# Kernel optimization log

Measured on AMD Instinct MI355X. Metric: run time of the kernel, lower is better.

Reference implementation:

```python
import jax, jax.numpy as jnp
import numpy as np

N = 20000       # nodes
E = 640000      # edges
H = 128         # hidden_nf = input_nf = output_nf = d_model = d_inner (expand=1)
D_STATE = 64
D_CONV = 4
DT_RANK = 8     # ceil(d_model/16) = ceil(128/16)


def setup_inputs() -> dict:
    key = jax.random.key(0)
    ks = jax.random.split(key, 20)
    g = lambda k, shape, s=0.05: jax.random.normal(k, shape, jnp.float32) * s
    return {
        'h': g(ks[0], (N, H), 1.0),
        'coord': g(ks[1], (N, 3), 1.0),
        'edge_index': jax.random.randint(ks[2], (2, E), 0, N),
        # edge_mlp: Linear(2H+1,H) ReLU Linear(H,H) ReLU
        'W_e1': g(ks[3], (H, 2 * H + 1)), 'b_e1': jnp.zeros(H, jnp.float32),
        'W_e2': g(ks[4], (H, H)), 'b_e2': jnp.zeros(H, jnp.float32),
        # att_mlp: Linear(H,1) + sigmoid
        'w_att': g(ks[5], (1, H)), 'b_att': jnp.zeros(1, jnp.float32),
        # node_mlp: Linear(2H,H) ReLU Linear(H,H)
        'W_n1': g(ks[6], (H, 2 * H)), 'b_n1': jnp.zeros(H, jnp.float32),
        'W_n2': g(ks[7], (H, H)), 'b_n2': jnp.zeros(H, jnp.float32),
        # coord_mlp: Linear(H,H) ReLU Linear(H,1,bias=False) (xavier gain 0.001)
        'W_c1': g(ks[8], (H, H)), 'b_c1': jnp.zeros(H, jnp.float32),
        'W_c2': g(ks[9], (1, H), 0.001),
        # pre_norm LayerNorm
        'ln_g': jnp.ones(H, jnp.float32), 'ln_b': jnp.zeros(H, jnp.float32),
        # Mamba(d_model=H, d_state=64, d_conv=4, expand=1)
        'in_proj_w': g(ks[10], (2 * H, H)),
        'conv_w': g(ks[11], (H, D_CONV), 0.2), 'conv_b': jnp.zeros(H, jnp.float32),
        'x_proj_w': g(ks[12], (DT_RANK + 2 * D_STATE, H)),
        'dt_proj_w': g(ks[13], (H, DT_RANK)), 'dt_proj_b': jnp.full((H,), -4.0, jnp.float32),
        'A_log': jnp.log(jnp.broadcast_to(jnp.arange(1, D_STATE + 1, dtype=jnp.float32), (H, D_STATE))),
        'D_skip': jnp.ones(H, jnp.float32),
        'out_proj_w': g(ks[14], (H, H)),
    }


def _layernorm(x, g, b):
    mu = jnp.mean(x, -1, keepdims=True)
    var = jnp.mean((x - mu) ** 2, -1, keepdims=True)
    return (x - mu) / jnp.sqrt(var + 1e-5) * g + b


def _mamba(x, in_proj_w, conv_w, conv_b, x_proj_w, dt_proj_w, dt_proj_b, A_log, D_skip, out_proj_w):
    # x: [L, H] treated as batch-1 sequence
    L = x.shape[0]
    xz = x @ in_proj_w.T                       # [L, 2H]
    u, z = xz[:, :H], xz[:, H:]
    # causal depthwise conv1d, kernel D_CONV
    up = jnp.pad(u, ((D_CONV - 1, 0), (0, 0)))
    uc = conv_b + sum(up[k:k + L] * conv_w[:, k] for k in range(D_CONV))
    uc = jax.nn.silu(uc)                       # [L, H]
    x_dbl = uc @ x_proj_w.T                    # [L, dt_rank + 2*d_state]
    dt = jax.nn.softplus(x_dbl[:, :DT_RANK] @ dt_proj_w.T + dt_proj_b)  # [L, H]
    Bm = x_dbl[:, DT_RANK:DT_RANK + D_STATE]   # [L, d_state]
    Cm = x_dbl[:, DT_RANK + D_STATE:]          # [L, d_state]
    A = -jnp.exp(A_log)                        # [H, d_state]

    def step(s, inp):
        dt_t, b_t, c_t, u_t = inp
        s = jnp.exp(dt_t[:, None] * A) * s + (dt_t * u_t)[:, None] * b_t[None, :]
        y = jnp.sum(s * c_t[None, :], -1) + D_skip * u_t
        return s, y

    _, ys = jax.lax.scan(step, jnp.zeros((H, D_STATE), jnp.float32), (dt, Bm, Cm, uc))
    y = ys * jax.nn.silu(z)
    return y @ out_proj_w.T


def reference(h, coord, edge_index, W_e1, b_e1, W_e2, b_e2, w_att, b_att,
              W_n1, b_n1, W_n2, b_n2, W_c1, b_c1, W_c2, ln_g, ln_b,
              in_proj_w, conv_w, conv_b, x_proj_w, dt_proj_w, dt_proj_b,
              A_log, D_skip, out_proj_w):
    e0, e1 = edge_index[0], edge_index[1]
    # coord2radial (norm_diff=False)
    coord_diff = coord[e0] - coord[e1]                         # [E, 3]
    radial = jnp.sum(coord_diff ** 2, 1, keepdims=True)        # [E, 1]
    # edge_model: hi = x[e0], hj = x[e1]; cat([hj, hi, radial])
    x_edge = jnp.concatenate([h[e1], h[e0], radial], axis=1)   # [E, 2H+1]
    mij = jax.nn.relu(jax.nn.relu(x_edge @ W_e1.T + b_e1) @ W_e2.T + b_e2)
    att = jax.nn.sigmoid(mij @ w_att.T + b_att)
    edge_feat = mij * att
    mi = jax.ops.segment_sum(edge_feat, e0, num_segments=N)    # [N, H]
    # coord_model (segment mean over e0)
    t = jax.nn.relu(edge_feat @ W_c1.T + b_c1) @ W_c2.T        # [E, 1]
    trans = jnp.clip(coord_diff * t, -100.0, 100.0)
    s = jax.ops.segment_sum(trans, e0, num_segments=N)
    cnt = jax.ops.segment_sum(jnp.ones_like(trans), e0, num_segments=N)
    coord_new = coord + (s / jnp.maximum(cnt, 1.0)) * 1.0      # coords_weight=1
    # node_mlp + pre_norm + clamp
    hn = jnp.concatenate([mi, h], axis=-1)
    hn = jax.nn.relu(hn @ W_n1.T + b_n1) @ W_n2.T + b_n2
    hn = _layernorm(hn, ln_g, ln_b)
    hn = jnp.clip(hn, -10.0, 10.0)
    # mamba over node sequence (bi=False, dropout=0, mamba_mlp=False)
    out = _mamba(hn, in_proj_w, conv_w, conv_b, x_proj_w, dt_proj_w,
                 dt_proj_b, A_log, D_skip, out_proj_w)
    return out, coord_new
```

## Files before the change

kernel.cpp:

```cpp
#include <hip/hip_runtime.h>
#include <math.h>

#define NN 20000
#define EE 640000
#define HD 128
#define NC 160
#define CS 125

typedef unsigned short ushort_t;
typedef __attribute__((ext_vector_type(8))) short short8v;
typedef __attribute__((ext_vector_type(4))) float f32x4;

#define MFMA16(a,b,c) __builtin_amdgcn_mfma_f32_16x16x32_bf16(a,b,c,0,0,0)

__device__ __forceinline__ float sigf(float x) { return 1.0f / (1.0f + __expf(-x)); }

__device__ __forceinline__ ushort_t f2b(float x) {
    unsigned u = __builtin_bit_cast(unsigned, x);
    unsigned r = (u + 0x7FFFu + ((u >> 16) & 1u)) >> 16;
    return (ushort_t)r;
}
__device__ __forceinline__ float b2f(ushort_t u) {
    unsigned v = ((unsigned)u) << 16;
    return __builtin_bit_cast(float, v);
}
__device__ __forceinline__ void splitf(float v, ushort_t& h, ushort_t& l) {
    h = f2b(v);
    l = f2b(v - b2f(h));
}
__device__ __forceinline__ void cvt8x2(const float* p, short8v& hi, short8v& lo) {
    #pragma unroll
    for (int j = 0; j < 8; ++j) {
        float v = p[j];
        ushort_t h, l; splitf(v, h, l);
        hi[j] = (short)h; lo[j] = (short)l;
    }
}

__global__ __launch_bounds__(1024) void prefix_kernel(const int* __restrict__ hist,
                                                      int* __restrict__ baseI)
{
    __shared__ int wsum[16];
    const int tid = threadIdx.x, lane = tid & 63, wid = tid >> 6;
    const int PER = 20;
    int i0 = tid * PER;
    int s = 0;
    for (int k = 0; k < PER; ++k) { int i = i0 + k; if (i < NN) s += hist[i]; }
    int v = s;
    #pragma unroll
    for (int off = 1; off < 64; off <<= 1) {
        int t = __shfl_up(v, off);
        if (lane >= off) v += t;
    }
    if (lane == 63) wsum[wid] = v;
    __syncthreads();
    if (tid == 0) {
        int acc = 0;
        #pragma unroll
        for (int w = 0; w < 16; ++w) { int t = wsum[w]; wsum[w] = acc; acc += t; }
    }
    __syncthreads();
    int excl = v - s + wsum[wid];
    for (int k = 0; k < PER; ++k) {
        int i = i0 + k;
        if (i < NN) { baseI[i] = excl; excl += hist[i]; }
    }
}

__global__ __launch_bounds__(256) void scatter_kernel(const int* __restrict__ ei,
                                                      const int* __restrict__ baseI,
                                                      int* __restrict__ cursor,
                                                      int* __restrict__ perm)
{
    int i = blockIdx.x * 256 + threadIdx.x;
    if (i < EE) {
        int n = ei[i];
        int p = baseI[n] + atomicAdd(&cursor[n], 1);
        perm[p] = i;
    }
}

__global__ __launch_bounds__(256) void prep_hist_kernel(
    const int* __restrict__ ei, int* __restrict__ histI,
    const float* __restrict__ We1, const float* __restrict__ We2,
    const float* __restrict__ Wc1, const float* __restrict__ Wn1,
    const float* __restrict__ Wn2, const float* __restrict__ Wip,
    const float* __restrict__ Wxp, const float* __restrict__ Wdt,
    const float* __restrict__ Wop,
    ushort_t* __restrict__ W12b, ushort_t* __restrict__ We2b,
    ushort_t* __restrict__ Wc1b,
    ushort_t* __restrict__ Wn1hi, ushort_t* __restrict__ Wn1lo,
    ushort_t* __restrict__ Wn2hi, ushort_t* __restrict__ Wn2lo,
    ushort_t* __restrict__ Wiphi, ushort_t* __restrict__ Wiplo,
    ushort_t* __restrict__ Wxp8hi, ushort_t* __restrict__ Wxp8lo,
    ushort_t* __restrict__ Wdt2hi, ushort_t* __restrict__ Wdt2lo,
    ushort_t* __restrict__ Wophi, ushort_t* __restrict__ Woplo)
{
    int i = blockIdx.x * 256 + threadIdx.x;
    if (i < EE) atomicAdd(&histI[ei[i]], 1);
    if (i < 256 * 128) {
        int j = i >> 7, k = i & 127;
        W12b[i] = f2b(We1[(j & 127) * 257 + ((j >> 7) << 7) + k]);
        ushort_t h, l;
        splitf(Wn1[i], h, l); Wn1hi[i] = h; Wn1lo[i] = l;
        splitf(Wip[i], h, l); Wiphi[i] = h; Wiplo[i] = l;
    }
    if (i < 128 * 128) {
        We2b[i] = f2b(We2[i]);
        Wc1b[i] = f2b(Wc1[i]);
        ushort_t h, l;
        splitf(Wn2[i], h, l); Wn2hi[i] = h; Wn2lo[i] = l;
        splitf(Wop[i], h, l); Wophi[i] = h; Woplo[i] = l;
        int j = i >> 7, k = i & 127;
        splitf(Wxp[(8 + j) * 128 + k], h, l); Wxp8hi[i] = h; Wxp8lo[i] = l;
        float s = 0.f;
        #pragma unroll
        for (int r = 0; r < 8; ++r) s = fmaf(Wdt[j * 8 + r], Wxp[r * 128 + k], s);
        splitf(s, h, l); Wdt2hi[i] = h; Wdt2lo[i] = l;
    }
}

__global__ __launch_bounds__(256) void p12_kernel(
    const float* __restrict__ h, const ushort_t* __restrict__ W12b,
    ushort_t* __restrict__ P12b)
{
    const int tid = threadIdx.x;
    const int lane = tid & 63;
    const int wid = tid >> 6;
    const int wm = wid >> 1, wn = wid & 1;
    const int g = lane >> 4, r16 = lane & 15;
    const int rbase = blockIdx.x * 128 + wm * 64;

    f32x4 acc[4][8];
    #pragma unroll
    for (int mt = 0; mt < 4; ++mt)
        #pragma unroll
        for (int nt = 0; nt < 8; ++nt) acc[mt][nt] = (f32x4){0.f, 0.f, 0.f, 0.f};

    for (int c = 0; c < 4; ++c) {
        short8v afr[4], bfr[8];
        #pragma unroll
        for (int mt = 0; mt < 4; ++mt) {
            int row = rbase + mt * 16 + r16;
            if (row > NN - 1) row = NN - 1;
            const float* p = h + (size_t)row * HD + c * 32 + g * 8;
            #pragma unroll
            for (int j = 0; j < 8; ++j) afr[mt][j] = (short)f2b(p[j]);
        }
        #pragma unroll
        for (int nt = 0; nt < 8; ++nt)
            bfr[nt] = *(const short8v*)(W12b + (size_t)(wn * 128 + nt * 16 + r16) * 128 + c * 32 + g * 8);
        #pragma unroll
        for (int mt = 0; mt < 4; ++mt)
            #pragma unroll
            for (int nt = 0; nt < 8; ++nt)
                acc[mt][nt] = MFMA16(afr[mt], bfr[nt], acc[mt][nt]);
    }
    #pragma unroll
    for (int mt = 0; mt < 4; ++mt)
        #pragma unroll
        for (int nt = 0; nt < 8; ++nt)
            #pragma unroll
            for (int r = 0; r < 4; ++r) {
                int row = rbase + mt * 16 + g * 4 + r;
                if (row < NN)
                    P12b[(size_t)row * 256 + wn * 128 + nt * 16 + r16] = f2b(acc[mt][nt][r]);
            }
}

__global__ __launch_bounds__(256) void edge_mfma(
    const ushort_t* __restrict__ P12b, const float* __restrict__ coord,
    const int* __restrict__ ei, const int* __restrict__ perm,
    const float* __restrict__ We1, const float* __restrict__ be1,
    const ushort_t* __restrict__ We2b, const float* __restrict__ be2,
    const float* __restrict__ watt, const float* __restrict__ batt,
    const ushort_t* __restrict__ Wc1b, const float* __restrict__ bc1,
    const float* __restrict__ Wc2,
    float* __restrict__ mi, float* __restrict__ ssum)
{
    __shared__ ushort_t ybuf[128 * 128];
    __shared__ float cdp[128][3];
    __shared__ float wcols[128], be1s[128], be2s[128], bc1s[128], watts[128], wc2s[128];
    __shared__ float pq[2][128];
    __shared__ int ej0s[128];

    const int tid = threadIdx.x;
    const int ebase = blockIdx.x * 128;
    const int lane = tid & 63;
    const int wid = tid >> 6;
    const int wm = wid >> 1, wn = wid & 1;
    const int g = lane >> 4, r16 = lane & 15;
    const float batt0 = batt[0];

    const int e = tid >> 1, hf = tid & 1;
    const int eg = perm[ebase + e];
    const int n0 = ei[eg];
    const int n1 = ei[EE + eg];
    {
        const ushort_t* p1 = P12b + (size_t)n1 * 256 + hf * 64;
        #pragma unroll
        for (int q = 0; q < 8; ++q) {
            short8v t = *(const short8v*)(p1 + q * 8);
            int off = (e << 8) + ((hf * 128 + q * 16) ^ ((e & 15) << 4));
            *(short8v*)((char*)ybuf + off) = t;
        }
    }
    if (hf == 0) ej0s[e] = n0;
    {
        int t = tid & 127;
        if (tid < 128) {
            wcols[t] = We1[t * 257 + 256];
            be1s[t] = be1[t];
            be2s[t] = be2[t];
        } else {
            bc1s[t] = bc1[t];
            watts[t] = watt[t];
            wc2s[t] = Wc2[t];
        }
    }
    float rr;
    {
        float d0 = coord[n0 * 3 + 0] - coord[n1 * 3 + 0];
        float d1 = coord[n0 * 3 + 1] - coord[n1 * 3 + 1];
        float d2 = coord[n0 * 3 + 2] - coord[n1 * 3 + 2];
        rr = d0 * d0 + d1 * d1 + d2 * d2;
        if (hf == 0) { cdp[e][0] = d0; cdp[e][1] = d1; cdp[e][2] = d2; }
    }
    __syncthreads();

    {
        short8v gb[8];
        const ushort_t* p2 = P12b + (size_t)n0 * 256 + 128 + hf * 64;
        #pragma unroll
        for (int q = 0; q < 8; ++q)
            gb[q] = *(const short8v*)(p2 + q * 8);
        const int colbase = hf * 64;
        #pragma unroll
        for (int q = 0; q < 8; ++q) {
            int off = (e << 8) + ((colbase * 2 + q * 16) ^ ((e & 15) << 4));
            short8v a = *(const short8v*)((const char*)ybuf + off);
            short8v ov;
            #pragma unroll
            for (int jj = 0; jj < 8; ++jj) {
                int col = colbase + q * 8 + jj;
                float v = b2f((ushort_t)a[jj]) + b2f((ushort_t)gb[q][jj]) + rr * wcols[col] + be1s[col];
                ov[jj] = (short)f2b(fmaxf(v, 0.f));
            }
            *(short8v*)((char*)ybuf + off) = ov;
        }
    }
    short8v b2_[4][4];
    {
        const ushort_t* W2p = We2b + (size_t)(wn * 64 + r16) * 128 + g * 8;
        #pragma unroll
        for (int nt = 0; nt < 4; ++nt)
            #pragma unroll
            for (int c = 0; c < 4; ++c)
                b2_[nt][c] = *(const short8v*)(W2p + nt * 2048 + c * 32);
    }
    __syncthreads();

    f32x4 acc[4][4];
    #pragma unroll
    for (int mt = 0; mt < 4; ++mt)
        #pragma unroll
        for (int nt = 0; nt < 4; ++nt) acc[mt][nt] = (f32x4){0.f, 0.f, 0.f, 0.f};
    #pragma unroll
    for (int c = 0; c < 4; ++c) {
        short8v afr[4];
        #pragma unroll
        for (int mt = 0; mt < 4; ++mt) {
            int row = wm * 64 + mt * 16 + r16;
            afr[mt] = *(const short8v*)((const char*)ybuf + (row << 8) + ((c * 64 + g * 16) ^ (r16 << 4)));
        }
        #pragma unroll
        for (int mt = 0; mt < 4; ++mt)
            #pragma unroll
            for (int nt = 0; nt < 4; ++nt)
                acc[mt][nt] = MFMA16(afr[mt], b2_[nt][c], acc[mt][nt]);
    }

    {
        float p[4][4];
        #pragma unroll
        for (int mt = 0; mt < 4; ++mt)
            #pragma unroll
            for (int r = 0; r < 4; ++r) p[mt][r] = 0.f;
        #pragma unroll
        for (int mt = 0; mt < 4; ++mt)
            #pragma unroll
            for (int nt = 0; nt < 4; ++nt)
                #pragma unroll
                for (int r = 0; r < 4; ++r) {
                    int col = wn * 64 + nt * 16 + r16;
                    float v = fmaxf(acc[mt][nt][r] + be2s[col], 0.f);
                    acc[mt][nt][r] = v;
                    p[mt][r] += v * watts[col];
                }
        #pragma unroll
        for (int off = 1; off < 16; off <<= 1)
            #pragma unroll
            for (int mt = 0; mt < 4; ++mt)
                #pragma unroll
                for (int r = 0; r < 4; ++r) p[mt][r] += __shfl_xor(p[mt][r], off);
        if (r16 == 0) {
            #pragma unroll
            for (int mt = 0; mt < 4; ++mt)
                #pragma unroll
                for (int r = 0; r < 4; ++r)
                    pq[wn][wm * 64 + mt * 16 + g * 4 + r] = p[mt][r];
        }
        __syncthreads();
        float att[4][4];
        #pragma unroll
        for (int mt = 0; mt < 4; ++mt)
            #pragma unroll
            for (int r = 0; r < 4; ++r) {
                int row = wm * 64 + mt * 16 + g * 4 + r;
                att[mt][r] = sigf(pq[0][row] + pq[1][row] + batt0);
            }
        __syncthreads();
        #pragma unroll
        for (int mt = 0; mt < 4; ++mt)
            #pragma unroll
            for (int nt = 0; nt < 4; ++nt)
                #pragma unroll
                for (int r = 0; r < 4; ++r) {
                    int row = wm * 64 + mt * 16 + g * 4 + r;
                    int col = wn * 64 + nt * 16 + r16;
                    int off = (row << 8) + (((col << 1)) ^ ((row & 15) << 4));
                    *(ushort_t*)((char*)ybuf + off) = f2b(acc[mt][nt][r] * att[mt][r]);
                }
    }
    __syncthreads();

    short8v b3_[4][4];
    {
        const ushort_t* W3p = Wc1b + (size_t)(wn * 64 + r16) * 128 + g * 8;
        #pragma unroll
        for (int nt = 0; nt < 4; ++nt)
            #pragma unroll
            for (int c = 0; c < 4; ++c)
                b3_[nt][c] = *(const short8v*)(W3p + nt * 2048 + c * 32);
    }

    {
        const int cp = tid & 63;
        const int qr = tid >> 6;
        const int r0 = qr * 32, r1 = r0 + 32;
        const int colbyte = cp * 4;
        float s0 = 0.f, s1 = 0.f;
        int cur = ej0s[r0];
        for (int r = r0; r < r1; ++r) {
            int node = ej0s[r];
            if (node != cur) {
                atomicAdd(&mi[(size_t)cur * HD + 2 * cp], s0);
                atomicAdd(&mi[(size_t)cur * HD + 2 * cp + 1], s1);
                s0 = 0.f; s1 = 0.f; cur = node;
            }
            int off = (r << 8) + (colbyte ^ ((r & 15) << 4));
            unsigned v = *(const unsigned*)((const char*)ybuf + off);
            s0 += b2f((ushort_t)(v & 0xFFFFu));
            s1 += b2f((ushort_t)(v >> 16));
        }
        atomicAdd(&mi[(size_t)cur * HD + 2 * cp], s0);
        atomicAdd(&mi[(size_t)cur * HD + 2 * cp + 1], s1);
    }

    #pragma unroll
    for (int mt = 0; mt < 4; ++mt)
        #pragma unroll
        for (int nt = 0; nt < 4; ++nt) acc[mt][nt] = (f32x4){0.f, 0.f, 0.f, 0.f};
    #pragma unroll
    for (int c = 0; c < 4; ++c) {
        short8v afr[4];
        #pragma unroll
        for (int mt = 0; mt < 4; ++mt) {
            int row = wm * 64 + mt * 16 + r16;
            afr[mt] = *(const short8v*)((const char*)ybuf + (row << 8) + ((c * 64 + g * 16) ^ (r16 << 4)));
        }
        #pragma unroll
        for (int mt = 0; mt < 4; ++mt)
            #pragma unroll
            for (int nt = 0; nt < 4; ++nt)
                acc[mt][nt] = MFMA16(afr[mt], b3_[nt][c], acc[mt][nt]);
    }
    {
        float q[4][4];
        #pragma unroll
        for (int mt = 0; mt < 4; ++mt)
            #pragma unroll
            for (int r = 0; r < 4; ++r) q[mt][r] = 0.f;
        #pragma unroll
        for (int mt = 0; mt < 4; ++mt)
            #pragma unroll
            for (int nt = 0; nt < 4; ++nt)
                #pragma unroll
                for (int r = 0; r < 4; ++r) {
                    int col = wn * 64 + nt * 16 + r16;
                    float v = fmaxf(acc[mt][nt][r] + bc1s[col], 0.f);
                    q[mt][r] += v * wc2s[col];
                }
        #pragma unroll
        for (int off = 1; off < 16; off <<= 1)
            #pragma unroll
            for (int mt = 0; mt < 4; ++mt)
                #pragma unroll
                for (int r = 0; r < 4; ++r) q[mt][r] += __shfl_xor(q[mt][r], off);
        if (r16 == 0) {
            #pragma unroll
            for (int mt = 0; mt < 4; ++mt)
                #pragma unroll
                for (int r = 0; r < 4; ++r)
                    pq[wn][wm * 64 + mt * 16 + g * 4 + r] = q[mt][r];
        }
        __syncthreads();
        if (tid < 48) {
            int c = tid % 3, seg = tid / 3;
            int r0 = seg * 8, r1 = r0 + 8;
            float sacc = 0.f; int cur = ej0s[r0];
            for (int r = r0; r < r1; ++r) {
                int node = ej0s[r];
                if (node != cur) {
                    atomicAdd(&ssum[cur * 3 + c], sacc);
                    sacc = 0.f; cur = node;
                }
                float tv = pq[0][r] + pq[1][r];
                float tr = cdp[r][c] * tv;
                tr = fminf(fmaxf(tr, -100.f), 100.f);
                sacc += tr;
            }
            atomicAdd(&ssum[cur * 3 + c], sacc);
        }
    }
}

__global__ __launch_bounds__(256) void node_mfma(
    const float* __restrict__ mi, const float* __restrict__ h,
    const ushort_t* __restrict__ Wn1hi, const ushort_t* __restrict__ Wn1lo,
    const float* __restrict__ bn1,
    const ushort_t* __restrict__ Wn2hi, const ushort_t* __restrict__ Wn2lo,
    const float* __restrict__ bn2,
    const float* __restrict__ lng, const float* __restrict__ lnb,
    const ushort_t* __restrict__ Wiphi, const ushort_t* __restrict__ Wiplo,
    ushort_t* __restrict__ ub, float* __restrict__ zs,
    const float* __restrict__ coord, const float* __restrict__ ssum,
    const int* __restrict__ histI, float* __restrict__ coordout)
{
    __shared__ ushort_t yhi[128 * 128];
    __shared__ ushort_t ylo[128 * 128];
    __shared__ float bn1s[128], bn2s[128], lngs[128], lnbs[128];

    const int tid = threadIdx.x;
    const int nbase = blockIdx.x * 128;
    const int lane = tid & 63;
    const int wid = tid >> 6;
    const int wm = wid >> 1, wn = wid & 1;
    const int g = lane >> 4, r16 = lane & 15;

    if (tid < 128) { bn1s[tid] = bn1[tid]; bn2s[tid] = bn2[tid]; lngs[tid] = lng[tid]; lnbs[tid] = lnb[tid]; }
    __syncthreads();

    f32x4 acc[4][4];
    #pragma unroll
    for (int mt = 0; mt < 4; ++mt)
        #pragma unroll
        for (int nt = 0; nt < 4; ++nt) acc[mt][nt] = (f32x4){0.f, 0.f, 0.f, 0.f};
    for (int c = 0; c < 8; ++c) {
        short8v ahi[4], alo[4], bhi[4], blo[4];
        #pragma unroll
        for (int mt = 0; mt < 4; ++mt) {
            int row = nbase + wm * 64 + mt * 16 + r16;
            if (row > NN - 1) row = NN - 1;
            const float* src = (c < 4) ? (mi + (size_t)row * HD + c * 32 + g * 8)
                                       : (h + (size_t)row * HD + (c - 4) * 32 + g * 8);
            cvt8x2(src, ahi[mt], alo[mt]);
        }
        #pragma unroll
        for (int nt = 0; nt < 4; ++nt) {
            size_t wo = (size_t)(wn * 64 + nt * 16 + r16) * 256 + c * 32 + g * 8;
            bhi[nt] = *(const short8v*)(Wn1hi + wo);
            blo[nt] = *(const short8v*)(Wn1lo + wo);
        }
        #pragma unroll
        for (int mt = 0; mt < 4; ++mt)
            #pragma unroll
            for (int nt = 0; nt < 4; ++nt) {
                acc[mt][nt] = MFMA16(ahi[mt], bhi[nt], acc[mt][nt]);
                acc[mt][nt] = MFMA16(ahi[mt], blo[nt], acc[mt][nt]);
                acc[mt][nt] = MFMA16(alo[mt], bhi[nt], acc[mt][nt]);
            }
    }
    #pragma unroll
    for (int mt = 0; mt < 4; ++mt)
        #pragma unroll
        for (int nt = 0; nt < 4; ++nt)
            #pragma unroll
            for (int r = 0; r < 4; ++r) {
                int row = wm * 64 + mt * 16 + g * 4 + r;
                int col = wn * 64 + nt * 16 + r16;
                int off = (row << 8) + (((col << 1)) ^ ((row & 15) << 4));
                float v = fmaxf(acc[mt][nt][r] + bn1s[col], 0.f);
                ushort_t hh, ll; splitf(v, hh, ll);
                *(ushort_t*)((char*)yhi + off) = hh;
                *(ushort_t*)((char*)ylo + off) = ll;
            }
    __syncthreads();

    #pragma unroll
    for (int mt = 0; mt < 4; ++mt)
        #pragma unroll
        for (int nt = 0; nt < 4; ++nt) acc[mt][nt] = (f32x4){0.f, 0.f, 0.f, 0.f};
    #pragma unroll
    for (int c = 0; c < 4; ++c) {
        short8v ahi[4], alo[4], bhi[4], blo[4];
        #pragma unroll
        for (int mt = 0; mt < 4; ++mt) {
            int row = wm * 64 + mt * 16 + r16;
            int off = (row << 8) + ((c * 64 + g * 16) ^ (r16 << 4));
            ahi[mt] = *(const short8v*)((const char*)yhi + off);
            alo[mt] = *(const short8v*)((const char*)ylo + off);
        }
        #pragma unroll
        for (int nt = 0; nt < 4; ++nt) {
            size_t wo = (size_t)(wn * 64 + nt * 16 + r16) * 128 + c * 32 + g * 8;
            bhi[nt] = *(const short8v*)(Wn2hi + wo);
            blo[nt] = *(const short8v*)(Wn2lo + wo);
        }
        #pragma unroll
        for (int mt = 0; mt < 4; ++mt)
            #pragma unroll
            for (int nt = 0; nt < 4; ++nt) {
                acc[mt][nt] = MFMA16(ahi[mt], bhi[nt], acc[mt][nt]);
                acc[mt][nt] = MFMA16(ahi[mt], blo[nt], acc[mt][nt]);
                acc[mt][nt] = MFMA16(alo[mt], bhi[nt], acc[mt][nt]);
            }
    }
    __syncthreads();
    #pragma unroll
    for (int mt = 0; mt < 4; ++mt)
        #pragma unroll
        for (int nt = 0; nt < 4; ++nt)
            #pragma unroll
            for (int r = 0; r < 4; ++r) {
                int row = wm * 64 + mt * 16 + g * 4 + r;
                int col = wn * 64 + nt * 16 + r16;
                int off = (row << 8) + (((col << 1)) ^ ((row & 15) << 4));
                float v = acc[mt][nt][r] + bn2s[col];
                ushort_t hh, ll; splitf(v, hh, ll);
                *(ushort_t*)((char*)yhi + off) = hh;
                *(ushort_t*)((char*)ylo + off) = ll;
            }
    __syncthreads();

    {
        const int row = tid >> 1, hf = tid & 1;
        float s1 = 0.f, s2 = 0.f;
        float vals[64];
        #pragma unroll
        for (int q = 0; q < 8; ++q) {
            int c8 = hf * 8 + q;
            int off = (row << 8) + ((c8 * 16) ^ ((row & 15) << 4));
            short8v vh = *(const short8v*)((const char*)yhi + off);
            short8v vl = *(const short8v*)((const char*)ylo + off);
            #pragma unroll
            for (int j = 0; j < 8; ++j) {
                float v = b2f((ushort_t)vh[j]) + b2f((ushort_t)vl[j]);
                vals[q * 8 + j] = v;
                s1 += v; s2 += v * v;
            }
        }
        s1 += __shfl_xor(s1, 1);
        s2 += __shfl_xor(s2, 1);
        float mu = s1 * (1.f / HD);
        float var = s2 * (1.f / HD) - mu * mu;
        float rs = rsqrtf(fmaxf(var, 0.f) + 1e-5f);
        #pragma unroll
        for (int q = 0; q < 8; ++q) {
            int c8 = hf * 8 + q;
            short8v oh, ol;
            #pragma unroll
            for (int j = 0; j < 8; ++j) {
                int col = c8 * 8 + j;
                float v = (vals[q * 8 + j] - mu) * rs * lngs[col] + lnbs[col];
                v = fminf(fmaxf(v, -10.f), 10.f);
                ushort_t hh, ll; splitf(v, hh, ll);
                oh[j] = (short)hh; ol[j] = (short)ll;
            }
            int off = (row << 8) + ((c8 * 16) ^ ((row & 15) << 4));
            *(short8v*)((char*)yhi + off) = oh;
            *(short8v*)((char*)ylo + off) = ol;
        }
    }

    {
        int base3 = nbase * 3;
        for (int k = tid; k < 384; k += 256) {
            int idx = base3 + k;
            if (idx < NN * 3) {
                int n = idx / 3;
                coordout[idx] = coord[idx] + ssum[idx] / fmaxf((float)histI[n], 1.f);
            }
        }
    }
    __syncthreads();

    #pragma unroll
    for (int jh = 0; jh < 2; ++jh) {
        #pragma unroll
        for (int mt = 0; mt < 4; ++mt)
            #pragma unroll
            for (int nt = 0; nt < 4; ++nt) acc[mt][nt] = (f32x4){0.f, 0.f, 0.f, 0.f};
        #pragma unroll
        for (int c = 0; c < 4; ++c) {
            short8v ahi[4], alo[4], bhi[4], blo[4];
            #pragma unroll
            for (int mt = 0; mt < 4; ++mt) {
                int row = wm * 64 + mt * 16 + r16;
                int off = (row << 8) + ((c * 64 + g * 16) ^ (r16 << 4));
                ahi[mt] = *(const short8v*)((const char*)yhi + off);
                alo[mt] = *(const short8v*)((const char*)ylo + off);
            }
            #pragma unroll
            for (int nt = 0; nt < 4; ++nt) {
                int j = wn * 128 + jh * 64 + nt * 16 + r16;
                size_t wo = (size_t)j * 128 + c * 32 + g * 8;
                bhi[nt] = *(const short8v*)(Wiphi + wo);
                blo[nt] = *(const short8v*)(Wiplo + wo);
            }
            #pragma unroll
            for (int mt = 0; mt < 4; ++mt)
                #pragma unroll
                for (int nt = 0; nt < 4; ++nt) {
                    acc[mt][nt] = MFMA16(ahi[mt], bhi[nt], acc[mt][nt]);
                    acc[mt][nt] = MFMA16(ahi[mt], blo[nt], acc[mt][nt]);
                    acc[mt][nt] = MFMA16(alo[mt], bhi[nt], acc[mt][nt]);
                }
        }
        #pragma unroll
        for (int mt = 0; mt < 4; ++mt)
            #pragma unroll
            for (int nt = 0; nt < 4; ++nt)
                #pragma unroll
                for (int r = 0; r < 4; ++r) {
                    int row = nbase + wm * 64 + mt * 16 + g * 4 + r;
                    if (row >= NN) continue;
                    int j = wn * 128 + jh * 64 + nt * 16 + r16;
                    float v = acc[mt][nt][r];
                    if (j < HD) ub[(size_t)row * HD + j] = f2b(v);
                    else        zs[(size_t)row * HD + (j - HD)] = v * sigf(v);
                }
    }
}

__global__ __launch_bounds__(256) void convdt_mfma(
    const ushort_t* __restrict__ ub, const float* __restrict__ cw,
    const float* __restrict__ cb,
    const ushort_t* __restrict__ Wxp8hi, const ushort_t* __restrict__ Wxp8lo,
    const ushort_t* __restrict__ Wdt2hi, const ushort_t* __restrict__ Wdt2lo,
    const float* __restrict__ bdt,
    float* __restrict__ uc, float* __restrict__ Bm, float* __restrict__ Cm,
    float* __restrict__ dt)
{
    __shared__ ushort_t yhi[128 * 128];
    __shared__ ushort_t ylo[128 * 128];
    __shared__ float cws[128][4], cbs[128], bdts[128];

    const int tid = threadIdx.x;
    const int nbase = blockIdx.x * 128;
    const int lane = tid & 63;
    const int wid = tid >> 6;
    const int wm = wid >> 1, wn = wid & 1;
    const int g = lane >> 4, r16 = lane & 15;

    if (tid < 128) {
        cbs[tid] = cb[tid]; bdts[tid] = bdt[tid];
        #pragma unroll
        for (int k = 0; k < 4; ++k) cws[tid][k] = cw[tid * 4 + k];
    }
    __syncthreads();

    for (int it = tid; it < 128 * 16; it += 256) {
        int r = it >> 4, cg = it & 15;
        int t = nbase + r;
        int colb = cg * 8;
        float a[8];
        #pragma unroll
        for (int j = 0; j < 8; ++j) a[j] = cbs[colb + j];
        #pragma unroll
        for (int k = 0; k < 4; ++k) {
            int tt = t - 3 + k;
            if (tt >= 0 && tt < NN) {
                short8v uv = *(const short8v*)(ub + (size_t)tt * HD + colb);
                #pragma unroll
                for (int j = 0; j < 8; ++j) a[j] = fmaf(b2f((ushort_t)uv[j]), cws[colb + j][k], a[j]);
            }
        }
        short8v oh, ol;
        f32x4 u0, u1;
        #pragma unroll
        for (int j = 0; j < 8; ++j) {
            float s = (t < NN) ? a[j] * sigf(a[j]) : 0.f;
            ushort_t hh, ll; splitf(s, hh, ll);
            oh[j] = (short)hh; ol[j] = (short)ll;
            if (j < 4) u0[j] = s; else u1[j - 4] = s;
        }
        int off = (r << 8) + ((cg * 16) ^ ((r & 15) << 4));
        *(short8v*)((char*)yhi + off) = oh;
        *(short8v*)((char*)ylo + off) = ol;
        if (t < NN) {
            *(f32x4*)(uc + (size_t)t * HD + colb) = u0;
            *(f32x4*)(uc + (size_t)t * HD + colb + 4) = u1;
        }
    }
    __syncthreads();

    f32x4 acc[4][4];
    #pragma unroll
    for (int mt = 0; mt < 4; ++mt)
        #pragma unroll
        for (int nt = 0; nt < 4; ++nt) acc[mt][nt] = (f32x4){0.f, 0.f, 0.f, 0.f};
    #pragma unroll
    for (int c = 0; c < 4; ++c) {
        short8v ahi[4], alo[4], bhi[4], blo[4];
        #pragma unroll
        for (int mt = 0; mt < 4; ++mt) {
            int row = wm * 64 + mt * 16 + r16;
            int off = (row << 8) + ((c * 64 + g * 16) ^ (r16 << 4));
            ahi[mt] = *(const short8v*)((const char*)yhi + off);
            alo[mt] = *(const short8v*)((const char*)ylo + off);
        }
        #pragma unroll
        for (int nt = 0; nt < 4; ++nt) {
            size_t wo = (size_t)(wn * 64 + nt * 16 + r16) * 128 + c * 32 + g * 8;
            bhi[nt] = *(const short8v*)(Wxp8hi + wo);
            blo[nt] = *(const short8v*)(Wxp8lo + wo);
        }
        #pragma unroll
        for (int mt = 0; mt < 4; ++mt)
            #pragma unroll
            for (int nt = 0; nt < 4; ++nt) {
                acc[mt][nt] = MFMA16(ahi[mt], bhi[nt], acc[mt][nt]);
                acc[mt][nt] = MFMA16(ahi[mt], blo[nt], acc[mt][nt]);
                acc[mt][nt] = MFMA16(alo[mt], bhi[nt], acc[mt][nt]);
            }
    }
    #pragma unroll
    for (int mt = 0; mt < 4; ++mt)
        #pragma unroll
        for (int nt = 0; nt < 4; ++nt)
            #pragma unroll
            for (int r = 0; r < 4; ++r) {
                int row = nbase + wm * 64 + mt * 16 + g * 4 + r;
                if (row >= NN) continue;
                int j = wn * 64 + nt * 16 + r16;
                float v = acc[mt][nt][r];
                if (j < 64) Bm[(size_t)row * 64 + j] = v;
                else        Cm[(size_t)row * 64 + (j - 64)] = v;
            }

    #pragma unroll
    for (int mt = 0; mt < 4; ++mt)
        #pragma unroll
        for (int nt = 0; nt < 4; ++nt) acc[mt][nt] = (f32x4){0.f, 0.f, 0.f, 0.f};
    #pragma unroll
    for (int c = 0; c < 4; ++c) {
        short8v ahi[4], alo[4], bhi[4], blo[4];
        #pragma unroll
        for (int mt = 0; mt < 4; ++mt) {
            int row = wm * 64 + mt * 16 + r16;
            int off = (row << 8) + ((c * 64 + g * 16) ^ (r16 << 4));
            ahi[mt] = *(const short8v*)((const char*)yhi + off);
            alo[mt] = *(const short8v*)((const char*)ylo + off);
        }
        #pragma unroll
        for (int nt = 0; nt < 4; ++nt) {
            size_t wo = (size_t)(wn * 64 + nt * 16 + r16) * 128 + c * 32 + g * 8;
            bhi[nt] = *(const short8v*)(Wdt2hi + wo);
            blo[nt] = *(const short8v*)(Wdt2lo + wo);
        }
        #pragma unroll
        for (int mt = 0; mt < 4; ++mt)
            #pragma unroll
            for (int nt = 0; nt < 4; ++nt) {
                acc[mt][nt] = MFMA16(ahi[mt], bhi[nt], acc[mt][nt]);
                acc[mt][nt] = MFMA16(ahi[mt], blo[nt], acc[mt][nt]);
                acc[mt][nt] = MFMA16(alo[mt], bhi[nt], acc[mt][nt]);
            }
    }
    #pragma unroll
    for (int mt = 0; mt < 4; ++mt)
        #pragma unroll
        for (int nt = 0; nt < 4; ++nt)
            #pragma unroll
            for (int r = 0; r < 4; ++r) {
                int row = nbase + wm * 64 + mt * 16 + g * 4 + r;
                if (row >= NN) continue;
                int j = wn * 64 + nt * 16 + r16;
                float a = acc[mt][nt][r] + bdts[j];
                float sp = (a > 20.f) ? a : log1pf(__expf(a));
                dt[(size_t)row * HD + j] = sp;
            }
}

__global__ __launch_bounds__(256) void scan1_kernel(
    const float* __restrict__ dt, const float* __restrict__ uc,
    const float* __restrict__ Bm, const float* __restrict__ Alog,
    float* __restrict__ cP, float* __restrict__ cS)
{
    int g = blockIdx.x * 256 + threadIdx.x;
    int c = g >> 12;
    int r = g & 4095;
    int hh = r >> 5;
    int dp = (r & 31) * 2;
    float A0 = -__expf(Alog[hh * 64 + dp]);
    float A1 = -__expf(Alog[hh * 64 + dp + 1]);
    float P0 = 1.f, S0 = 0.f, P1 = 1.f, S1 = 0.f;
    int t0 = c * CS;
    for (int t = t0; t < t0 + CS; ++t) {
        float dtv = dt[t * HD + hh];
        float uv = uc[t * HD + hh];
        float du = dtv * uv;
        float2 bv = *(const float2*)(Bm + (size_t)t * 64 + dp);
        float a0 = __expf(dtv * A0);
        float a1 = __expf(dtv * A1);
        P0 *= a0; P1 *= a1;
        S0 = fmaf(a0, S0, du * bv.x);
        S1 = fmaf(a1, S1, du * bv.y);
    }
    *(float2*)(cP + (size_t)c * 8192 + hh * 64 + dp) = make_float2(P0, P1);
    *(float2*)(cS + (size_t)c * 8192 + hh * 64 + dp) = make_float2(S0, S1);
}

__global__ __launch_bounds__(256) void scan2_kernel(
    const float* __restrict__ cP, const float* __restrict__ cS, float* __restrict__ cI)
{
    int g = blockIdx.x * 256 + threadIdx.x;
    float S = 0.f;
    for (int c = 0; c < NC; ++c) {
        cI[c * 8192 + g] = S;
        S = fmaf(cP[c * 8192 + g], S, cS[c * 8192 + g]);
    }
}

__global__ __launch_bounds__(256) void scan3_kernel(
    const float* __restrict__ dt, const float* __restrict__ uc,
    const float* __restrict__ Bm, const float* __restrict__ Cm,
    const float* __restrict__ Alog, const float* __restrict__ Dskip,
    const float* __restrict__ cI, float* __restrict__ y)
{
    int g = blockIdx.x * 256 + threadIdx.x;
    int c = g >> 12;
    int r = g & 4095;
    int hh = r >> 5;
    int dp = (r & 31) * 2;
    float A0 = -__expf(Alog[hh * 64 + dp]);
    float A1 = -__expf(Alog[hh * 64 + dp + 1]);
    float s0 = cI[c * 8192 + hh * 64 + dp];
    float s1 = cI[c * 8192 + hh * 64 + dp + 1];
    float Dh = Dskip[hh];
    int t0 = c * CS;
    const int lane31 = threadIdx.x & 31;
    for (int t = t0; t < t0 + CS; ++t) {
        float dtv = dt[t * HD + hh];
        float uv = uc[t * HD + hh];
        float du = dtv * uv;
        float2 bv = *(const float2*)(Bm + (size_t)t * 64 + dp);
        float2 cv = *(const float2*)(Cm + (size_t)t * 64 + dp);
        s0 = fmaf(__expf(dtv * A0), s0, du * bv.x);
        s1 = fmaf(__expf(dtv * A1), s1, du * bv.y);
        float yp = fmaf(s0, cv.x, s1 * cv.y);
        #pragma unroll
        for (int off = 1; off < 32; off <<= 1) yp += __shfl_xor(yp, off);
        if (lane31 == 0) y[t * HD + hh] = yp + Dh * uv;
    }
}

__global__ __launch_bounds__(256) void out_mfma(
    const float* __restrict__ y, const float* __restrict__ zs,
    const ushort_t* __restrict__ Wophi, const ushort_t* __restrict__ Woplo,
    float* __restrict__ outp)
{
    const int tid = threadIdx.x;
    const int lane = tid & 63;
    const int wid = tid >> 6;
    const int wm = wid >> 1, wn = wid & 1;
    const int g = lane >> 4, r16 = lane & 15;
    const int nbase = blockIdx.x * 128;

    f32x4 acc[4][4];
    #pragma unroll
    for (int mt = 0; mt < 4; ++mt)
        #pragma unroll
        for (int nt = 0; nt < 4; ++nt) acc[mt][nt] = (f32x4){0.f, 0.f, 0.f, 0.f};

    for (int c = 0; c < 4; ++c) {
        short8v ahi[4], alo[4], bhi[4], blo[4];
        #pragma unroll
        for (int mt = 0; mt < 4; ++mt) {
            int row = nbase + wm * 64 + mt * 16 + r16;
            if (row > NN - 1) row = NN - 1;
            const float* yp = y + (size_t)row * HD + c * 32 + g * 8;
            const float* zp = zs + (size_t)row * HD + c * 32 + g * 8;
            #pragma unroll
            for (int j = 0; j < 8; ++j) {
                float v = yp[j] * zp[j];
                ushort_t hh, ll; splitf(v, hh, ll);
                ahi[mt][j] = (short)hh; alo[mt][j] = (short)ll;
            }
        }
        #pragma unroll
        for (int nt = 0; nt < 4; ++nt) {
            size_t wo = (size_t)(wn * 64 + nt * 16 + r16) * 128 + c * 32 + g * 8;
            bhi[nt] = *(const short8v*)(Wophi + wo);
            blo[nt] = *(const short8v*)(Woplo + wo);
        }
        #pragma unroll
        for (int mt = 0; mt < 4; ++mt)
            #pragma unroll
            for (int nt = 0; nt < 4; ++nt) {
                acc[mt][nt] = MFMA16(ahi[mt], bhi[nt], acc[mt][nt]);
                acc[mt][nt] = MFMA16(ahi[mt], blo[nt], acc[mt][nt]);
                acc[mt][nt] = MFMA16(alo[mt], bhi[nt], acc[mt][nt]);
            }
    }
    #pragma unroll
    for (int mt = 0; mt < 4; ++mt)
        #pragma unroll
        for (int nt = 0; nt < 4; ++nt)
            #pragma unroll
            for (int r = 0; r < 4; ++r) {
                int row = nbase + wm * 64 + mt * 16 + g * 4 + r;
                if (row < NN)
                    outp[(size_t)row * HD + wn * 64 + nt * 16 + r16] = acc[mt][nt][r];
            }
}

extern "C" void kernel_launch(void* const* d_in, const int* in_sizes, int n_in,
                              void* d_out, int out_size, void* d_ws, size_t ws_size,
                              hipStream_t stream)
{
    const float* h     = (const float*)d_in[0];
    const float* coord = (const float*)d_in[1];
    const int*   ei    = (const int*)d_in[2];
    const float* We1   = (const float*)d_in[3];
    const float* be1   = (const float*)d_in[4];
    const float* We2   = (const float*)d_in[5];
    const float* be2   = (const float*)d_in[6];
    const float* watt  = (const float*)d_in[7];
    const float* batt  = (const float*)d_in[8];
    const float* Wn1   = (const float*)d_in[9];
    const float* bn1   = (const float*)d_in[10];
    const float* Wn2   = (const float*)d_in[11];
    const float* bn2   = (const float*)d_in[12];
    const float* Wc1   = (const float*)d_in[13];
    const float* bc1   = (const float*)d_in[14];
    const float* Wc2   = (const float*)d_in[15];
    const float* lng   = (const float*)d_in[16];
    const float* lnb   = (const float*)d_in[17];
    const float* Wip   = (const float*)d_in[18];
    const float* convw = (const float*)d_in[19];
    const float* convb = (const float*)d_in[20];
    const float* Wxp   = (const float*)d_in[21];
    const float* Wdt   = (const float*)d_in[22];
    const float* bdt   = (const float*)d_in[23];
    const float* Alog  = (const float*)d_in[24];
    const float* Dskip = (const float*)d_in[25];
    const float* Wop   = (const float*)d_in[26];

    float* ws   = (float*)d_ws;
    float* mi   = ws;
    float* ssum = mi   + (size_t)NN * HD;
    int*   histI  = (int*)(ssum + (size_t)NN * 3);
    int*   cursor = histI + NN;
    int*   baseI  = cursor + NN;
    int*   perm   = baseI + NN;
    float* zsb  = (float*)(perm + EE);
    float* ucb  = zsb  + (size_t)NN * HD;
    float* dtb  = ucb  + (size_t)NN * HD;
    float* Bm   = dtb  + (size_t)NN * HD;
    float* Cm   = Bm   + (size_t)NN * 64;
    float* cP   = Cm   + (size_t)NN * 64;
    float* cSb  = cP   + (size_t)NC * 8192;
    float* cIb  = cSb  + (size_t)NC * 8192;
    ushort_t* ub    = (ushort_t*)(cIb + (size_t)NC * 8192);
    ushort_t* W12bp = ub + (size_t)NN * HD;
    ushort_t* We2bp = W12bp + 256 * 128;
    ushort_t* Wc1bp = We2bp + 128 * 128;
    ushort_t* Wn1hi = Wc1bp + 128 * 128;
    ushort_t* Wn1lo = Wn1hi + 128 * 256;
    ushort_t* Wn2hi = Wn1lo + 128 * 256;
    ushort_t* Wn2lo = Wn2hi + 128 * 128;
    ushort_t* Wiphi = Wn2lo + 128 * 128;
    ushort_t* Wiplo = Wiphi + 256 * 128;
    ushort_t* Wxp8hi = Wiplo + 256 * 128;
    ushort_t* Wxp8lo = Wxp8hi + 128 * 128;
    ushort_t* Wdt2hi = Wxp8lo + 128 * 128;
    ushort_t* Wdt2lo = Wdt2hi + 128 * 128;
    ushort_t* Wophi  = Wdt2lo + 128 * 128;
    ushort_t* Woplo  = Wophi + 128 * 128;
    ushort_t* P12bp = (ushort_t*)cP;
    float* yb = mi;

    float* outp     = (float*)d_out;
    float* coordout = outp + (size_t)NN * HD;

    hipMemsetAsync(ws, 0, (size_t)NN * 133 * 4, stream);

    prep_hist_kernel<<<(EE + 255) / 256, 256, 0, stream>>>(ei, histI,
                                         We1, We2, Wc1, Wn1, Wn2, Wip, Wxp, Wdt, Wop,
                                         W12bp, We2bp, Wc1bp,
                                         Wn1hi, Wn1lo, Wn2hi, Wn2lo, Wiphi, Wiplo,
                                         Wxp8hi, Wxp8lo, Wdt2hi, Wdt2lo, Wophi, Woplo);
    prefix_kernel<<<1, 1024, 0, stream>>>(histI, baseI);
    scatter_kernel<<<(EE + 255) / 256, 256, 0, stream>>>(ei, baseI, cursor, perm);
    p12_kernel<<<(NN + 127) / 128, 256, 0, stream>>>(h, W12bp, P12bp);
    edge_mfma<<<EE / 128, 256, 0, stream>>>(P12bp, coord, ei, perm, We1, be1,
                                            We2bp, be2, watt, batt, Wc1bp, bc1, Wc2,
                                            mi, ssum);
    node_mfma<<<(NN + 127) / 128, 256, 0, stream>>>(mi, h, Wn1hi, Wn1lo, bn1,
                                                    Wn2hi, Wn2lo, bn2, lng, lnb,
                                                    Wiphi, Wiplo, ub, zsb,
                                                    coord, ssum, histI, coordout);
    convdt_mfma<<<(NN + 127) / 128, 256, 0, stream>>>(ub, convw, convb,
                                                      Wxp8hi, Wxp8lo, Wdt2hi, Wdt2lo,
                                                      bdt, ucb, Bm, Cm, dtb);
    scan1_kernel<<<NC * 4096 / 256, 256, 0, stream>>>(dtb, ucb, Bm, Alog, cP, cSb);
    scan2_kernel<<<8192 / 256, 256, 0, stream>>>(cP, cSb, cIb);
    scan3_kernel<<<NC * 4096 / 256, 256, 0, stream>>>(dtb, ucb, Bm, Cm, Alog, Dskip, cIb, yb);
    out_mfma<<<(NN + 127) / 128, 256, 0, stream>>>(yb, zsb, Wophi, Woplo, outp);
}
```

Baseline: 639.5 us.

## Halve edge tile to 64 edges per block and stream weight fragments

The edge MLP kernel now processes 64 edges per block instead of 128, with four threads per edge for the gather. Each wave computes a 32x64 output tile. Weight B fragments are loaded from global memory inside the k-loop instead of being preloaded into registers. The segment-sum of mi is reorganized to one column per thread over 32 rows. The aim is to cut shared memory and register pressure to raise occupancy, at the cost of twice as many blocks, more redundant weight loads, and more atomics at block boundaries.

```diff
diff --git a/kernel.cpp b/kernel.cpp
--- a/kernel.cpp
+++ b/kernel.cpp
@@ -178,34 +178,34 @@
     const float* __restrict__ Wc2,
     float* __restrict__ mi, float* __restrict__ ssum)
 {
-    __shared__ ushort_t ybuf[128 * 128];
-    __shared__ float cdp[128][3];
+    __shared__ ushort_t ybuf[64 * 128];
+    __shared__ float cdp[64][3];
     __shared__ float wcols[128], be1s[128], be2s[128], bc1s[128], watts[128], wc2s[128];
-    __shared__ float pq[2][128];
-    __shared__ int ej0s[128];
+    __shared__ float pq[2][64];
+    __shared__ int ej0s[64];
 
     const int tid = threadIdx.x;
-    const int ebase = blockIdx.x * 128;
+    const int ebase = blockIdx.x * 64;
     const int lane = tid & 63;
     const int wid = tid >> 6;
     const int wm = wid >> 1, wn = wid & 1;
     const int g = lane >> 4, r16 = lane & 15;
     const float batt0 = batt[0];
 
-    const int e = tid >> 1, hf = tid & 1;
+    const int e = tid >> 2, qf = tid & 3;
     const int eg = perm[ebase + e];
     const int n0 = ei[eg];
     const int n1 = ei[EE + eg];
     {
-        const ushort_t* p1 = P12b + (size_t)n1 * 256 + hf * 64;
-        #pragma unroll
-        for (int q = 0; q < 8; ++q) {
+        const ushort_t* p1 = P12b + (size_t)n1 * 256 + qf * 32;
+        #pragma unroll
+        for (int q = 0; q < 4; ++q) {
             short8v t = *(const short8v*)(p1 + q * 8);
-            int off = (e << 8) + ((hf * 128 + q * 16) ^ ((e & 15) << 4));
+            int off = (e << 8) + ((qf * 64 + q * 16) ^ ((e & 15) << 4));
             *(short8v*)((char*)ybuf + off) = t;
         }
     }
-    if (hf == 0) ej0s[e] = n0;
+    if (qf == 0) ej0s[e] = n0;
     {
         int t = tid & 127;
         if (tid < 128) {
@@ -224,19 +224,19 @@
         float d1 = coord[n0 * 3 + 1] - coord[n1 * 3 + 1];
         float d2 = coord[n0 * 3 + 2] - coord[n1 * 3 + 2];
         rr = d0 * d0 + d1 * d1 + d2 * d2;
-        if (hf == 0) { cdp[e][0] = d0; cdp[e][1] = d1; cdp[e][2] = d2; }
+        if (qf == 0) { cdp[e][0] = d0; cdp[e][1] = d1; cdp[e][2] = d2; }
     }
     __syncthreads();
 
     {
-        short8v gb[8];
-        const ushort_t* p2 = P12b + (size_t)n0 * 256 + 128 + hf * 64;
-        #pragma unroll
-        for (int q = 0; q < 8; ++q)
+        short8v gb[4];
+        const ushort_t* p2 = P12b + (size_t)n0 * 256 + 128 + qf * 32;
+        #pragma unroll
+        for (int q = 0; q < 4; ++q)
             gb[q] = *(const short8v*)(p2 + q * 8);
-        const int colbase = hf * 64;
-        #pragma unroll
-        for (int q = 0; q < 8; ++q) {
+        const int colbase = qf * 32;
+        #pragma unroll
+        for (int q = 0; q < 4; ++q) {
             int off = (e << 8) + ((colbase * 2 + q * 16) ^ ((e & 15) << 4));
             short8v a = *(const short8v*)((const char*)ybuf + off);
             short8v ov;
@@ -249,45 +249,39 @@
             *(short8v*)((char*)ybuf + off) = ov;
         }
     }
-    short8v b2_[4][4];
+    __syncthreads();
+
+    f32x4 acc[2][4];
+    #pragma unroll
+    for (int mt = 0; mt < 2; ++mt)
+        #pragma unroll
+        for (int nt = 0; nt < 4; ++nt) acc[mt][nt] = (f32x4){0.f, 0.f, 0.f, 0.f};
+    #pragma unroll
+    for (int c = 0; c < 4; ++c) {
+        short8v afr[2], bfr[4];
+        #pragma unroll
+        for (int mt = 0; mt < 2; ++mt) {
+            int row = wm * 32 + mt * 16 + r16;
+            afr[mt] = *(const short8v*)((const char*)ybuf + (row << 8) + ((c * 64 + g * 16) ^ (r16 << 4)));
+        }
+        #pragma unroll
+        for (int nt = 0; nt < 4; ++nt)
+            bfr[nt] = *(const short8v*)(We2b + (size_t)(wn * 64 + nt * 16 + r16) * 128 + c * 32 + g * 8);
+        #pragma unroll
+        for (int mt = 0; mt < 2; ++mt)
+            #pragma unroll
+            for (int nt = 0; nt < 4; ++nt)
+                acc[mt][nt] = MFMA16(afr[mt], bfr[nt], acc[mt][nt]);
+    }
+
     {
-        const ushort_t* W2p = We2b + (size_t)(wn * 64 + r16) * 128 + g * 8;
-        #pragma unroll
-        for (int nt = 0; nt < 4; ++nt)
-            #pragma unroll
-            for (int c = 0; c < 4; ++c)
-                b2_[nt][c] = *(const short8v*)(W2p + nt * 2048 + c * 32);
-    }
-    __syncthreads();
-
-    f32x4 acc[4][4];
-    #pragma unroll
-    for (int mt = 0; mt < 4; ++mt)
-        #pragma unroll
-        for (int nt = 0; nt < 4; ++nt) acc[mt][nt] = (f32x4){0.f, 0.f, 0.f, 0.f};
-    #pragma unroll
-    for (int c = 0; c < 4; ++c) {
-        short8v afr[4];
-        #pragma unroll
-        for (int mt = 0; mt < 4; ++mt) {
-            int row = wm * 64 + mt * 16 + r16;
-            afr[mt] = *(const short8v*)((const char*)ybuf + (row << 8) + ((c * 64 + g * 16) ^ (r16 << 4)));
-        }
-        #pragma unroll
-        for (int mt = 0; mt < 4; ++mt)
-            #pragma unroll
-            for (int nt = 0; nt < 4; ++nt)
-                acc[mt][nt] = MFMA16(afr[mt], b2_[nt][c], acc[mt][nt]);
-    }
-
-    {
-        float p[4][4];
-        #pragma unroll
-        for (int mt = 0; mt < 4; ++mt)
+        float p[2][4];
+        #pragma unroll
+        for (int mt = 0; mt < 2; ++mt)
             #pragma unroll
             for (int r = 0; r < 4; ++r) p[mt][r] = 0.f;
         #pragma unroll
-        for (int mt = 0; mt < 4; ++mt)
+        for (int mt = 0; mt < 2; ++mt)
             #pragma unroll
             for (int nt = 0; nt < 4; ++nt)
                 #pragma unroll
@@ -300,33 +294,33 @@
         #pragma unroll
         for (int off = 1; off < 16; off <<= 1)
             #pragma unroll
-            for (int mt = 0; mt < 4; ++mt)
+            for (int mt = 0; mt < 2; ++mt)
                 #pragma unroll
                 for (int r = 0; r < 4; ++r) p[mt][r] += __shfl_xor(p[mt][r], off);
         if (r16 == 0) {
             #pragma unroll
-            for (int mt = 0; mt < 4; ++mt)
+            for (int mt = 0; mt < 2; ++mt)
                 #pragma unroll
                 for (int r = 0; r < 4; ++r)
-                    pq[wn][wm * 64 + mt * 16 + g * 4 + r] = p[mt][r];
+                    pq[wn][wm * 32 + mt * 16 + g * 4 + r] = p[mt][r];
         }
         __syncthreads();
-        float att[4][4];
-        #pragma unroll
-        for (int mt = 0; mt < 4; ++mt)
+        float att[2][4];
+        #pragma unroll
+        for (int mt = 0; mt < 2; ++mt)
             #pragma unroll
             for (int r = 0; r < 4; ++r) {
-                int row = wm * 64 + mt * 16 + g * 4 + r;
+                int row = wm * 32 + mt * 16 + g * 4 + r;
                 att[mt][r] = sigf(pq[0][row] + pq[1][row] + batt0);
             }
         __syncthreads();
         #pragma unroll
-        for (int mt = 0; mt < 4; ++mt)
+        for (int mt = 0; mt < 2; ++mt)
             #pragma unroll
             for (int nt = 0; nt < 4; ++nt)
                 #pragma unroll
                 for (int r = 0; r < 4; ++r) {
-                    int row = wm * 64 + mt * 16 + g * 4 + r;
+                    int row = wm * 32 + mt * 16 + g * 4 + r;
                     int col = wn * 64 + nt * 16 + r16;
                     int off = (row << 8) + (((col << 1)) ^ ((row & 15) << 4));
                     *(ushort_t*)((char*)ybuf + off) = f2b(acc[mt][nt][r] * att[mt][r]);
@@ -334,65 +328,51 @@
     }
     __syncthreads();
 
-    short8v b3_[4][4];
     {
-        const ushort_t* W3p = Wc1b + (size_t)(wn * 64 + r16) * 128 + g * 8;
-        #pragma unroll
-        for (int nt = 0; nt < 4; ++nt)
-            #pragma unroll
-            for (int c = 0; c < 4; ++c)
-                b3_[nt][c] = *(const short8v*)(W3p + nt * 2048 + c * 32);
-    }
-
-    {
-        const int cp = tid & 63;
-        const int qr = tid >> 6;
-        const int r0 = qr * 32, r1 = r0 + 32;
-        const int colbyte = cp * 4;
-        float s0 = 0.f, s1 = 0.f;
-        int cur = ej0s[r0];
+        const int col = tid & 127, half = tid >> 7;
+        const int r0 = half * 32, r1 = r0 + 32;
+        float sacc = 0.f; int cur = ej0s[r0];
         for (int r = r0; r < r1; ++r) {
             int node = ej0s[r];
             if (node != cur) {
-                atomicAdd(&mi[(size_t)cur * HD + 2 * cp], s0);
-                atomicAdd(&mi[(size_t)cur * HD + 2 * cp + 1], s1);
-                s0 = 0.f; s1 = 0.f; cur = node;
-            }
-            int off = (r << 8) + (colbyte ^ ((r & 15) << 4));
-            unsigned v = *(const unsigned*)((const char*)ybuf + off);
-            s0 += b2f((ushort_t)(v & 0xFFFFu));
-            s1 += b2f((ushort_t)(v >> 16));
-        }
-        atomicAdd(&mi[(size_t)cur * HD + 2 * cp], s0);
-        atomicAdd(&mi[(size_t)cur * HD + 2 * cp + 1], s1);
-    }
-
-    #pragma unroll
-    for (int mt = 0; mt < 4; ++mt)
+                atomicAdd(&mi[(size_t)cur * HD + col], sacc);
+                sacc = 0.f; cur = node;
+            }
+            int off = (r << 8) + (((col << 1)) ^ ((r & 15) << 4));
+            sacc += b2f(*(const ushort_t*)((const char*)ybuf + off));
+        }
+        atomicAdd(&mi[(size_t)cur * HD + col], sacc);
+    }
+
+    #pragma unroll
+    for (int mt = 0; mt < 2; ++mt)
         #pragma unroll
         for (int nt = 0; nt < 4; ++nt) acc[mt][nt] = (f32x4){0.f, 0.f, 0.f, 0.f};
     #pragma unroll
     for (int c = 0; c < 4; ++c) {
-        short8v afr[4];
-        #pragma unroll
-        for (int mt = 0; mt < 4; ++mt) {
-            int row = wm * 64 + mt * 16 + r16;
+        short8v afr[2], bfr[4];
+        #pragma unroll
+        for (int mt = 0; mt < 2; ++mt) {
+            int row = wm * 32 + mt * 16 + r16;
             afr[mt] = *(const short8v*)((const char*)ybuf + (row << 8) + ((c * 64 + g * 16) ^ (r16 << 4)));
         }
         #pragma unroll
-        for (int mt = 0; mt < 4; ++mt)
+        for (int nt = 0; nt < 4; ++nt)
+            bfr[nt] = *(const short8v*)(Wc1b + (size_t)(wn * 64 + nt * 16 + r16) * 128 + c * 32 + g * 8);
+        #pragma unroll
+        for (int mt = 0; mt < 2; ++mt)
             #pragma unroll
             for (int nt = 0; nt < 4; ++nt)
-                acc[mt][nt] = MFMA16(afr[mt], b3_[nt][c], acc[mt][nt]);
+                acc[mt][nt] = MFMA16(afr[mt], bfr[nt], acc[mt][nt]);
     }
     {
-        float q[4][4];
-        #pragma unroll
-        for (int mt = 0; mt < 4; ++mt)
+        float q[2][4];
+        #pragma unroll
+        for (int mt = 0; mt < 2; ++mt)
             #pragma unroll
             for (int r = 0; r < 4; ++r) q[mt][r] = 0.f;
         #pragma unroll
-        for (int mt = 0; mt < 4; ++mt)
+        for (int mt = 0; mt < 2; ++mt)
             #pragma unroll
             for (int nt = 0; nt < 4; ++nt)
                 #pragma unroll
@@ -404,18 +384,18 @@
         #pragma unroll
         for (int off = 1; off < 16; off <<= 1)
             #pragma unroll
-            for (int mt = 0; mt < 4; ++mt)
+            for (int mt = 0; mt < 2; ++mt)
                 #pragma unroll
                 for (int r = 0; r < 4; ++r) q[mt][r] += __shfl_xor(q[mt][r], off);
         if (r16 == 0) {
             #pragma unroll
-            for (int mt = 0; mt < 4; ++mt)
+            for (int mt = 0; mt < 2; ++mt)
                 #pragma unroll
                 for (int r = 0; r < 4; ++r)
-                    pq[wn][wm * 64 + mt * 16 + g * 4 + r] = q[mt][r];
+                    pq[wn][wm * 32 + mt * 16 + g * 4 + r] = q[mt][r];
         }
         __syncthreads();
-        if (tid < 48) {
+        if (tid < 24) {
             int c = tid % 3, seg = tid / 3;
             int r0 = seg * 8, r1 = r0 + 8;
             float sacc = 0.f; int cur = ej0s[r0];
@@ -1015,9 +995,9 @@
     prefix_kernel<<<1, 1024, 0, stream>>>(histI, baseI);
     scatter_kernel<<<(EE + 255) / 256, 256, 0, stream>>>(ei, baseI, cursor, perm);
     p12_kernel<<<(NN + 127) / 128, 256, 0, stream>>>(h, W12bp, P12bp);
-    edge_mfma<<<EE / 128, 256, 0, stream>>>(P12bp, coord, ei, perm, We1, be1,
-                                            We2bp, be2, watt, batt, Wc1bp, bc1, Wc2,
-                                            mi, ssum);
+    edge_mfma<<<EE / 64, 256, 0, stream>>>(P12bp, coord, ei, perm, We1, be1,
+                                           We2bp, be2, watt, batt, Wc1bp, bc1, Wc2,
+                                           mi, ssum);
     node_mfma<<<(NN + 127) / 128, 256, 0, stream>>>(mi, h, Wn1hi, Wn1lo, bn1,
                                                     Wn2hi, Wn2lo, bn2, lng, lnb,
                                                     Wiphi, Wiplo, ub, zsb,
```

Measured after the change: 652.5 us. 2.0% more time.
